# Kernel optimization log

Hardware: AMD Instinct MI355X
Metric: run time of the kernel (lower is better)

The kernel has to match this reference:

```python
import jax, jax.numpy as jnp
import numpy as np

W_ENTROPY, W_MI, W_COV, W_ORTHO, W_L1, W_L2 = 1.0, 0.2, 0.2, 0.1, 0.1, 0.1


def setup_inputs() -> dict:
    key = jax.random.key(0)
    k1, k2, k3, k4 = jax.random.split(key, 4)
    B, NCLS, C = 16384, 1000, 1280
    logits = jax.random.normal(k1, (B, NCLS), dtype=jnp.float32)
    output = jax.nn.log_softmax(logits, axis=1)  # nll_loss expects log-probs
    target = jax.random.randint(k2, (B,), 0, NCLS, dtype=jnp.int64)
    weights = jax.random.normal(k3, (NCLS, C), dtype=jnp.float32) * 0.02
    features = jax.random.normal(k4, (B, C), dtype=jnp.float32)
    return {"output": output, "target": target, "weights": weights, "features": features}


def _kl_loss(features):
    # torch: sum_{i,j} F.kl_div(L[:, i], L[:, j], log_target=True, reduction='mean')
    # kl_div(input, tgt, log_target=True) = mean_b exp(tgt)*(tgt - input)
    # => sum_{i,j,b} P[b,j]*(L[b,j]-L[b,i]) / B
    #  = (C * sum(P*L) - sum(L)) / B   (since sum_j P[b,j] == 1)
    B, C = features.shape
    L = jax.nn.log_softmax(features, axis=1)
    P = jnp.exp(L)
    return (C * jnp.sum(P * L) - jnp.sum(L)) / B


def _cov_loss(features):
    B = features.shape[0]
    cf = features - jnp.mean(features, axis=0, keepdims=True)
    cov = (cf.T @ cf) / B  # [C, C]
    eye = jnp.eye(cov.shape[0], dtype=cov.dtype)
    return jnp.sum((cov - eye) ** 2)  # ||.||_F^2


def _ortho_loss(weights):
    w = weights.reshape(weights.shape[0], -1)
    cov = w @ w.T  # row type
    eye = jnp.eye(cov.shape[0], dtype=cov.dtype)
    return jnp.sum((cov - eye) ** 2)


def reference(output, target, weights, features):
    loss_nll = -jnp.mean(jnp.take_along_axis(output, target[:, None], axis=1))
    loss_kl = _kl_loss(features)
    loss_cov = _cov_loss(features)
    loss_ortho = _ortho_loss(weights)
    loss_l1 = jnp.sum(jnp.abs(weights))
    loss_l2 = jnp.sqrt(jnp.sum(weights ** 2))
    loss = (W_ENTROPY * loss_nll + W_MI * loss_kl + W_COV * loss_cov
            + W_ORTHO * loss_ortho + W_L1 * loss_l1 + W_L2 * loss_l2)
    return loss
```

## Files before the change

### kernel.cpp

```cpp
#include <hip/hip_runtime.h>
#include <stdint.h>
#include <stddef.h>

#define B_N    16384
#define NCLS_N 1000
#define C_N    1280

#define ACC_OFF    0ULL
#define TICKET_OFF 64ULL
#define COLSUM_OFF 128ULL
#define FBT_OFF    8192ULL
#define WB_OFF     41951232ULL
#define G_OFF      44572672ULL
#define H_OFF      51126272ULL
#define HP_OFF     102244352ULL
#define WS_PART_NEED 111681536ULL

enum { A_NLL = 0, A_KL = 1, A_L1 = 2, A_L2SQ = 3, A_SUMSQF = 4, A_FMU2 = 5, A_GFRO = 6, A_HFRO = 7 };

typedef short s16x8 __attribute__((ext_vector_type(8)));
typedef float f32x4 __attribute__((ext_vector_type(4)));

__device__ __forceinline__ unsigned short f2bf(float f) {
    union { float f; unsigned int u; } v; v.f = f;
    unsigned int u = v.u;
    u += 0x7fffu + ((u >> 16) & 1u);
    return (unsigned short)(u >> 16);
}

__device__ __forceinline__ float wave_red(float v) {
#pragma unroll
    for (int o = 32; o; o >>= 1) v += __shfl_down(v, o, 64);
    return v;
}


__device__ __forceinline__ void nll_body(const float* __restrict__ lp,
                                         const int* __restrict__ tgt,
                                         float* __restrict__ acc, int bidx) {
    int b = bidx * 256 + threadIdx.x;
    int t = tgt[b];
    float v = lp[(size_t)b * NCLS_N + t];
    v = wave_red(v);
    __shared__ float sm_nll[4];
    int wid = threadIdx.x >> 6, lane = threadIdx.x & 63;
    if (lane == 0) sm_nll[wid] = v;
    __syncthreads();
    if (threadIdx.x == 0) atomicAdd(&acc[A_NLL], sm_nll[0] + sm_nll[1] + sm_nll[2] + sm_nll[3]);
}

__device__ __forceinline__ void wpass_body(const float* __restrict__ W,
                                           short* __restrict__ Wb,
                                           float* __restrict__ acc, int idx) {
    int bx = idx & 3;
    int kc = idx >> 2;
    int m = bx * 256 + threadIdx.x;
    bool live = (m < NCLS_N);
    const float4* Wr = (const float4*)(W + (size_t)m * C_N);
    float l1 = 0.f, l2 = 0.f;
#pragma unroll
    for (int kj = 0; kj < 4; kj++) {
        s16x8 pk = { 0, 0, 0, 0, 0, 0, 0, 0 };
        if (live) {
            float4 a = Wr[kc * 8 + kj * 2];
            float4 b = Wr[kc * 8 + kj * 2 + 1];
            l1 += fabsf(a.x) + fabsf(a.y) + fabsf(a.z) + fabsf(a.w)
                + fabsf(b.x) + fabsf(b.y) + fabsf(b.z) + fabsf(b.w);
            l2 += a.x * a.x + a.y * a.y + a.z * a.z + a.w * a.w
                + b.x * b.x + b.y * b.y + b.z * b.z + b.w * b.w;
            pk[0] = (short)f2bf(a.x); pk[1] = (short)f2bf(a.y);
            pk[2] = (short)f2bf(a.z); pk[3] = (short)f2bf(a.w);
            pk[4] = (short)f2bf(b.x); pk[5] = (short)f2bf(b.y);
            pk[6] = (short)f2bf(b.z); pk[7] = (short)f2bf(b.w);
        }
        *(s16x8*)(Wb + ((size_t)(kc * 4 + kj) * 1024 + m) * 8) = pk;
    }
    l1 = wave_red(l1);
    l2 = wave_red(l2);
    __shared__ float sm_w[4][2];
    int wid = threadIdx.x >> 6, lane = threadIdx.x & 63;
    if (lane == 0) { sm_w[wid][0] = l1; sm_w[wid][1] = l2; }
    __syncthreads();
    if (threadIdx.x == 0) {
        atomicAdd(&acc[A_L1],   sm_w[0][0] + sm_w[1][0] + sm_w[2][0] + sm_w[3][0]);
        atomicAdd(&acc[A_L2SQ], sm_w[0][1] + sm_w[1][1] + sm_w[2][1] + sm_w[3][1]);
    }
}

__device__ __forceinline__ void fpass_body(const float* __restrict__ F,
                                           short* __restrict__ Fbt,
                                           float* __restrict__ colsum,
                                           float* __restrict__ acc, int idx) {
    int bx = idx % 5;
    int by = idx / 5;
    int c = bx * 256 + threadIdx.x;
    int kc0 = by * 4;
    float cs = 0.f, sq = 0.f;
    for (int ch = 0; ch < 4; ch++) {
        int kc = kc0 + ch;
        int kbase = kc * 32;
#pragma unroll
        for (int kj = 0; kj < 4; kj++) {
            float v[8];
#pragma unroll
            for (int e = 0; e < 8; e++) v[e] = F[(size_t)(kbase + kj * 8 + e) * C_N + c];
            s16x8 pk;
#pragma unroll
            for (int e = 0; e < 8; e++) {
                cs += v[e];
                sq += v[e] * v[e];
                pk[e] = (short)f2bf(v[e]);
            }
            *(s16x8*)(Fbt + ((size_t)(kc * 4 + kj) * C_N + c) * 8) = pk;
        }
    }
    atomicAdd(&colsum[c], cs);
    sq = wave_red(sq);
    __shared__ float sm_f[4];
    int wid = threadIdx.x >> 6, lane = threadIdx.x & 63;
    if (lane == 0) sm_f[wid] = sq;
    __syncthreads();
    if (threadIdx.x == 0) atomicAdd(&acc[A_SUMSQF], sm_f[0] + sm_f[1] + sm_f[2] + sm_f[3]);
}

__device__ __forceinline__ void klpass_body(const float* __restrict__ F,
                                            float* __restrict__ acc, int idx) {
    int wid = threadIdx.x >> 6, lane = threadIdx.x & 63;
    int gwave = idx * 4 + wid;
    float kl_acc = 0.f;
    for (int b = gwave; b < B_N; b += 4096) {
        const float4* Fr = (const float4*)(F + (size_t)b * C_N);
        float s = 0.f, tt = 0.f;
#pragma unroll
        for (int i = 0; i < 5; i++) {
            float4 f = Fr[lane + 64 * i];
            float e0 = __expf(f.x), e1 = __expf(f.y), e2 = __expf(f.z), e3 = __expf(f.w);
            s  += e0 + e1 + e2 + e3;
            tt += e0 * f.x + e1 * f.y + e2 * f.z + e3 * f.w;
        }
        s = wave_red(s); tt = wave_red(tt);
        if (lane == 0) kl_acc += (float)C_N * (tt / s);
    }
    __shared__ float sm_kl[4];
    if (lane == 0) sm_kl[wid] = kl_acc;
    __syncthreads();
    if (threadIdx.x == 0)
        atomicAdd(&acc[A_KL], sm_kl[0] + sm_kl[1] + sm_kl[2] + sm_kl[3]);
}

template<bool PART>
__device__ __forceinline__ void gram_body(const short* __restrict__ X,
                                          float* __restrict__ S,
                                          int Mp, int T, int ntri,
                                          int tile, int kc_blk, int k0step, int nt) {
    __shared__ __align__(16) short A0[128 * 32];
    __shared__ __align__(16) short A1[128 * 32];
    __shared__ __align__(16) short B0[128 * 32];
    __shared__ __align__(16) short B1[128 * 32];
    int tid = threadIdx.x;
    int bi = 0, rem = tile;
    while (rem >= T - bi) { rem -= T - bi; bi++; }
    int bj = bi + rem;
    int i0 = bi * 128, j0 = bj * 128;

    int wave = tid >> 6, lane = tid & 63;
    int wm = wave >> 1, wn = wave & 1;
    int quad = lane >> 4, l16 = lane & 15;

    const size_t kstep = (size_t)Mp * 32;
    const short *pa0, *pa1, *pb0, *pb1;
    int lo0 = tid * 8, lo1 = (256 + tid) * 8;
    {
        int g0 = tid, g1 = 256 + tid;
        int r0 = g0 >> 2, r1 = g1 >> 2;
        int kj0 = (g0 & 3) ^ (r0 & 3), kj1 = (g1 & 3) ^ (r1 & 3);
        size_t base = (size_t)k0step * kstep;
        pa0 = X + base + ((size_t)kj0 * Mp + i0 + r0) * 8;
        pa1 = X + base + ((size_t)kj1 * Mp + i0 + r1) * 8;
        pb0 = X + base + ((size_t)kj0 * Mp + j0 + r0) * 8;
        pb1 = X + base + ((size_t)kj1 * Mp + j0 + r1) * 8;
    }

    f32x4 acc[4][4];
#pragma unroll
    for (int i = 0; i < 4; i++)
#pragma unroll
        for (int j = 0; j < 4; j++) acc[i][j] = { 0.f, 0.f, 0.f, 0.f };

    auto stage = [&](short* Ad, short* Bd) {
        __builtin_amdgcn_global_load_lds((const __attribute__((address_space(1))) unsigned int*)pa0,
                                         (__attribute__((address_space(3))) unsigned int*)(Ad + lo0), 16, 0, 0);
        __builtin_amdgcn_global_load_lds((const __attribute__((address_space(1))) unsigned int*)pa1,
                                         (__attribute__((address_space(3))) unsigned int*)(Ad + lo1), 16, 0, 0);
        __builtin_amdgcn_global_load_lds((const __attribute__((address_space(1))) unsigned int*)pb0,
                                         (__attribute__((address_space(3))) unsigned int*)(Bd + lo0), 16, 0, 0);
        __builtin_amdgcn_global_load_lds((const __attribute__((address_space(1))) unsigned int*)pb1,
                                         (__attribute__((address_space(3))) unsigned int*)(Bd + lo1), 16, 0, 0);
        pa0 += kstep; pa1 += kstep; pb0 += kstep; pb1 += kstep;
    };

    auto compute = [&](const short* Ab, const short* Bb) {
        s16x8 af[4], bfr[4];
#pragma unroll
        for (int f = 0; f < 4; f++) {
            int mrow = wm * 64 + f * 16 + l16;
            af[f] = *(const s16x8*)(Ab + mrow * 32 + (quad ^ (mrow & 3)) * 8);
            int nrow = wn * 64 + f * 16 + l16;
            bfr[f] = *(const s16x8*)(Bb + nrow * 32 + (quad ^ (nrow & 3)) * 8);
        }
        __builtin_amdgcn_s_setprio(1);
#pragma unroll
        for (int i = 0; i < 4; i++)
#pragma unroll
            for (int j = 0; j < 4; j++)
                acc[i][j] = __builtin_amdgcn_mfma_f32_16x16x32_bf16(af[i], bfr[j], acc[i][j], 0, 0, 0);
        __builtin_amdgcn_s_setprio(0);
    };

    stage(A0, B0);
    __syncthreads();
    for (int t = 0; t < nt; t += 2) {
        stage(A1, B1);
        compute(A0, B0);
        __syncthreads();
        if (t + 2 < nt) stage(A0, B0);
        compute(A1, B1);
        __syncthreads();
    }

    if (PART) {
        float* Sp = S + (((size_t)kc_blk * ntri + tile) << 14);
#pragma unroll
        for (int i = 0; i < 4; i++)
#pragma unroll
            for (int j = 0; j < 4; j++)
#pragma unroll
                for (int r = 0; r < 4; r++) {
                    int lrow = wm * 64 + i * 16 + quad * 4 + r;
                    int lcol = wn * 64 + j * 16 + l16;
                    Sp[lrow * 128 + lcol] = acc[i][j][r];
                }
    } else {
#pragma unroll
        for (int i = 0; i < 4; i++)
#pragma unroll
            for (int j = 0; j < 4; j++)
#pragma unroll
                for (int r = 0; r < 4; r++) {
                    int grow = i0 + wm * 64 + i * 16 + quad * 4 + r;
                    int gcol = j0 + wn * 64 + j * 16 + l16;
                    atomicAdd(&S[(size_t)grow * Mp + gcol], acc[i][j][r]);
                }
    }
}

__device__ __forceinline__ void fro_tile_any(const float* __restrict__ S,
                                             const float* __restrict__ mu_src,
                                             int Mp, int T, int ntri, int tile, int nks, bool part,
                                             float* __restrict__ slotF,
                                             float* __restrict__ slotQ) {
    int bi = 0, rem = tile;
    while (rem >= T - bi) { rem -= T - bi; bi++; }
    int bj = bi + rem;
    size_t baseA = (size_t)bi * 128 * Mp + (size_t)bj * 128;
    const float* baseP = S + ((size_t)tile << 14);
    size_t pstride = (size_t)ntri << 14;
    const float invB = 1.f / (float)B_N;
    float sum = 0.f, q = 0.f;
    for (int l = threadIdx.x * 4; l < 128 * 128; l += 1024) {
        int row = l >> 7, col = l & 127;
        float4 v;
        if (part) {
            v = *(const float4*)(baseP + l);
            for (int ks = 1; ks < nks; ks++) {
                float4 u = *(const float4*)(baseP + (size_t)ks * pstride + l);
                v.x += u.x; v.y += u.y; v.z += u.z; v.w += u.w;
            }
        } else {
            v = *(const float4*)(S + baseA + (size_t)row * Mp + col);
        }
        sum += v.x * v.x + v.y * v.y + v.z * v.z + v.w * v.w;
        if (mu_src) {
            float mr = mu_src[bi * 128 + row] * invB;
            float4 mc = *(const float4*)(mu_src + bj * 128 + col);
            q += mr * (v.x * mc.x + v.y * mc.y + v.z * mc.z + v.w * mc.w) * invB;
        }
    }
    sum = wave_red(sum);
    q = wave_red(q);
    __shared__ float sm_fro[4][2];
    int wid = threadIdx.x >> 6, lane = threadIdx.x & 63;
    if (lane == 0) { sm_fro[wid][0] = sum; sm_fro[wid][1] = q; }
    __syncthreads();
    if (threadIdx.x == 0) {
        float w = (bi == bj) ? 1.f : 2.f;
        atomicAdd(slotF, w * (sm_fro[0][0] + sm_fro[1][0] + sm_fro[2][0] + sm_fro[3][0]));
        if (mu_src)
            atomicAdd(slotQ, w * (sm_fro[0][1] + sm_fro[1][1] + sm_fro[2][1] + sm_fro[3][1]));
    }
}


__global__ __launch_bounds__(256) void prep_kernel(const float* __restrict__ lp,
                                                   const int* __restrict__ tgt,
                                                   const float* __restrict__ W,
                                                   const float* __restrict__ F,
                                                   short* __restrict__ Wb,
                                                   short* __restrict__ Fbt,
                                                   float* __restrict__ colsum,
                                                   float* __restrict__ acc,
                                                   float* __restrict__ G,
                                                   float* __restrict__ H) {
    int b = blockIdx.x;
    if (b < 1024) {
        klpass_body(F, acc, b);
    } else if (b < 1664) {
        fpass_body(F, Fbt, colsum, acc, b - 1024);
    } else if (b < 1824) {
        wpass_body(W, Wb, acc, b - 1664);
    } else if (b < 1888) {
        nll_body(lp, tgt, acc, b - 1824);
    } else if (b < 1988) {
        float4* p = (float4*)G + (size_t)(b - 1888) * 4096;
        float4 z = { 0.f, 0.f, 0.f, 0.f };
        for (int i = threadIdx.x; i < 4096; i += 256) p[i] = z;
    } else {
        float4* p = (float4*)H + (size_t)(b - 1988) * 4096;
        float4 z = { 0.f, 0.f, 0.f, 0.f };
        for (int i = threadIdx.x; i < 4096; i += 256) p[i] = z;
    }
}

template<bool PART>
__global__ __launch_bounds__(256) void main_kernel(const short* __restrict__ Fbt,
                                                   float* __restrict__ G,
                                                   const short* __restrict__ Wb,
                                                   float* __restrict__ H) {
    const int G_NT[16] = {18,22,26,30,20,24,28,32,46,42,38,34,44,40,36,32};
    const int G_K0[16] = {0,18,40,66,96,116,140,168,200,246,288,326,360,404,444,480};
    const int H_NT[4]  = {8,10,12,10};
    const int H_K0[4]  = {0,8,18,30};
    int b = blockIdx.x;
    if (b < 880) {
        int tile = b >> 4, kc = b & 15;
        int k0 = PART ? kc * 32 : G_K0[kc];
        int nt = PART ? 32      : G_NT[kc];
        gram_body<PART>(Fbt, G, C_N, 10, 55, tile, kc, k0, nt);
    } else {
        int l = b - 880;
        int tile = l >> 2, kc = l & 3;
        int k0 = PART ? kc * 10 : H_K0[kc];
        int nt = PART ? 10      : H_NT[kc];
        gram_body<PART>(Wb, H, 1024, 8, 36, tile, kc, k0, nt);
    }
}

template<bool PART>
__global__ __launch_bounds__(256) void fro_final_kernel(const float* __restrict__ G,
                                                        const float* __restrict__ H,
                                                        float* __restrict__ acc,
                                                        const float* __restrict__ colsum,
                                                        unsigned* __restrict__ ticket,
                                                        float* __restrict__ out) {
    int b = blockIdx.x;
    if (b < 55) fro_tile_any(G, colsum, C_N, 10, 55, b, 16, PART, acc + A_GFRO, acc + A_FMU2);
    else        fro_tile_any(H, nullptr, 1024, 8, 36, b - 55, 4, PART, acc + A_HFRO, nullptr);

    __shared__ int amlast;
    if (threadIdx.x == 0) {
        __threadfence();
        unsigned prev = atomicAdd(ticket, 1u);
        amlast = (prev == 90u);
    }
    __syncthreads();
    if (!amlast) return;
    __threadfence();

    float s = 0.f, s1 = 0.f;
    for (int c = threadIdx.x; c < C_N; c += 256) { float v = colsum[c]; s += v * v; s1 += v; }
    s = wave_red(s);
    s1 = wave_red(s1);
    __shared__ float sm[4][2];
    int wid = threadIdx.x >> 6, lane = threadIdx.x & 63;
    if (lane == 0) { sm[wid][0] = s; sm[wid][1] = s1; }
    __syncthreads();
    if (threadIdx.x == 0) {
        double musq_raw = (double)(sm[0][0] + sm[1][0] + sm[2][0] + sm[3][0]);
        double sumF     = (double)(sm[0][1] + sm[1][1] + sm[2][1] + sm[3][1]);
        double Bd = (double)B_N;
        double gfro = (double)atomicAdd(&acc[A_GFRO], 0.0f);
        double hfro = (double)atomicAdd(&acc[A_HFRO], 0.0f);
        double fmu2 = (double)atomicAdd(&acc[A_FMU2], 0.0f);
        double nll = -((double)acc[A_NLL] / Bd);
        double kl  = ((double)acc[A_KL] - sumF) / Bd;
        double trG = (double)acc[A_SUMSQF];
        double musq = musq_raw / (Bd * Bd);
        double cov = gfro / (Bd * Bd)
                   - (2.0 / Bd) * fmu2
                   + musq * musq
                   - 2.0 * (trG / Bd - musq)
                   + (double)C_N;
        double ortho = hfro - 2.0 * (double)acc[A_L2SQ] + (double)NCLS_N;
        double loss = 1.0 * nll + 0.2 * kl + 0.2 * cov + 0.1 * ortho
                    + 0.1 * (double)acc[A_L1] + 0.1 * sqrt((double)acc[A_L2SQ]);
        out[0] = (float)loss;
    }
}

extern "C" void kernel_launch(void* const* d_in, const int* in_sizes, int n_in,
                              void* d_out, int out_size, void* d_ws, size_t ws_size,
                              hipStream_t stream) {
    (void)in_sizes; (void)n_in; (void)out_size;
    const float* output_lp = (const float*)d_in[0];
    const int*   target    = (const int*)d_in[1];
    const float* W         = (const float*)d_in[2];
    const float* F         = (const float*)d_in[3];

    char*     ws     = (char*)d_ws;
    float*    acc    = (float*)(ws + ACC_OFF);
    unsigned* ticket = (unsigned*)(ws + TICKET_OFF);
    float*    colsum = (float*)(ws + COLSUM_OFF);
    short*    Fbt    = (short*)(ws + FBT_OFF);
    short*    Wb     = (short*)(ws + WB_OFF);

    bool part = (ws_size >= WS_PART_NEED);

    hipMemsetAsync(ws, 0, 8192, stream);

    if (part) {
        float* Gp = (float*)(ws + G_OFF);
        float* Hp = (float*)(ws + HP_OFF);
        prep_kernel<<<1888, 256, 0, stream>>>(output_lp, target, W, F, Wb, Fbt, colsum, acc, Gp, Hp);
        main_kernel<true><<<1024, 256, 0, stream>>>(Fbt, Gp, Wb, Hp);
        fro_final_kernel<true><<<91, 256, 0, stream>>>(Gp, Hp, acc, colsum, ticket, (float*)d_out);
    } else {
        float* G = (float*)(ws + G_OFF);
        float* H = (float*)(ws + H_OFF);
        prep_kernel<<<2052, 256, 0, stream>>>(output_lp, target, W, F, Wb, Fbt, colsum, acc, G, H);
        main_kernel<false><<<1024, 256, 0, stream>>>(Fbt, G, Wb, H);
        fro_final_kernel<false><<<91, 256, 0, stream>>>(G, H, acc, colsum, ticket, (float*)d_out);
    }
}
```

Baseline: 268.5 us.

## Fuse KL and feature-transpose passes; split fro tiles into quarter-tile blocks

Merges the separate KL pass and the bf16 feature transpose/colsum pass into a single kernel body, so the 84 MB feature matrix is read once instead of twice. Each wave handles 8 rows with coalesced float4 loads, accumulates column sums in shared memory and writes the transposed bf16 layout. It also splits each Frobenius tile reduction into four 32-row blocks to raise parallelism in the final kernel, and adjusts the last-block ticket count to match. The costs are shared-memory atomics for column sums and more register pressure from per-row accumulators.

Result: no change. 266.2 us (-0.8%).

```diff
diff --git a/kernel.cpp b/kernel.cpp
--- a/kernel.cpp
+++ b/kernel.cpp
@@ -87,65 +87,66 @@
     }
 }
 
-__device__ __forceinline__ void fpass_body(const float* __restrict__ F,
-                                           short* __restrict__ Fbt,
-                                           float* __restrict__ colsum,
-                                           float* __restrict__ acc, int idx) {
-    int bx = idx % 5;
-    int by = idx / 5;
-    int c = bx * 256 + threadIdx.x;
-    int kc0 = by * 4;
-    float cs = 0.f, sq = 0.f;
-    for (int ch = 0; ch < 4; ch++) {
-        int kc = kc0 + ch;
-        int kbase = kc * 32;
-#pragma unroll
-        for (int kj = 0; kj < 4; kj++) {
-            float v[8];
-#pragma unroll
-            for (int e = 0; e < 8; e++) v[e] = F[(size_t)(kbase + kj * 8 + e) * C_N + c];
-            s16x8 pk;
-#pragma unroll
-            for (int e = 0; e < 8; e++) {
-                cs += v[e];
-                sq += v[e] * v[e];
-                pk[e] = (short)f2bf(v[e]);
-            }
-            *(s16x8*)(Fbt + ((size_t)(kc * 4 + kj) * C_N + c) * 8) = pk;
+__device__ __forceinline__ void fkpass_body(const float* __restrict__ F,
+                                            short* __restrict__ Fbt,
+                                            float* __restrict__ colsum,
+                                            float* __restrict__ acc, int kc) {
+    __shared__ float csum[C_N];
+    __shared__ float sm_red[4][2];
+    int tid = threadIdx.x;
+    int w = tid >> 6, lane = tid & 63;
+    for (int i = tid; i < C_N; i += 256) csum[i] = 0.f;
+    __syncthreads();
+
+    int b0 = kc * 32 + w * 8;
+    float s_acc[8], tt_acc[8];
+#pragma unroll
+    for (int r = 0; r < 8; r++) { s_acc[r] = 0.f; tt_acc[r] = 0.f; }
+    float sq = 0.f;
+
+    for (int cc = 0; cc < 5; cc++) {
+        int cbase = cc * 256 + 4 * lane;
+        f32x4 cs = { 0.f, 0.f, 0.f, 0.f };
+        s16x8 out0, out1, out2, out3;
+#pragma unroll
+        for (int r = 0; r < 8; r++) {
+            float4 f = *(const float4*)(F + (size_t)(b0 + r) * C_N + cbase);
+            float e0 = __expf(f.x), e1 = __expf(f.y), e2 = __expf(f.z), e3 = __expf(f.w);
+            s_acc[r]  += e0 + e1 + e2 + e3;
+            tt_acc[r] += e0 * f.x + e1 * f.y + e2 * f.z + e3 * f.w;
+            cs.x += f.x; cs.y += f.y; cs.z += f.z; cs.w += f.w;
+            sq += f.x * f.x + f.y * f.y + f.z * f.z + f.w * f.w;
+            out0[r] = (short)f2bf(f.x);
+            out1[r] = (short)f2bf(f.y);
+            out2[r] = (short)f2bf(f.z);
+            out3[r] = (short)f2bf(f.w);
         }
-    }
-    atomicAdd(&colsum[c], cs);
+        short* dst = Fbt + ((size_t)(kc * 4 + w) * C_N + cbase) * 8;
+        *(s16x8*)(dst)      = out0;
+        *(s16x8*)(dst + 8)  = out1;
+        *(s16x8*)(dst + 16) = out2;
+        *(s16x8*)(dst + 24) = out3;
+        atomicAdd(&csum[cbase + 0], cs.x);
+        atomicAdd(&csum[cbase + 1], cs.y);
+        atomicAdd(&csum[cbase + 2], cs.z);
+        atomicAdd(&csum[cbase + 3], cs.w);
+    }
+
+    float kl_acc = 0.f;
+#pragma unroll
+    for (int r = 0; r < 8; r++) {
+        float s = wave_red(s_acc[r]);
+        float tt = wave_red(tt_acc[r]);
+        if (lane == 0) kl_acc += (float)C_N * (tt / s);
+    }
     sq = wave_red(sq);
-    __shared__ float sm_f[4];
-    int wid = threadIdx.x >> 6, lane = threadIdx.x & 63;
-    if (lane == 0) sm_f[wid] = sq;
-    __syncthreads();
-    if (threadIdx.x == 0) atomicAdd(&acc[A_SUMSQF], sm_f[0] + sm_f[1] + sm_f[2] + sm_f[3]);
-}
-
-__device__ __forceinline__ void klpass_body(const float* __restrict__ F,
-                                            float* __restrict__ acc, int idx) {
-    int wid = threadIdx.x >> 6, lane = threadIdx.x & 63;
-    int gwave = idx * 4 + wid;
-    float kl_acc = 0.f;
-    for (int b = gwave; b < B_N; b += 4096) {
-        const float4* Fr = (const float4*)(F + (size_t)b * C_N);
-        float s = 0.f, tt = 0.f;
-#pragma unroll
-        for (int i = 0; i < 5; i++) {
-            float4 f = Fr[lane + 64 * i];
-            float e0 = __expf(f.x), e1 = __expf(f.y), e2 = __expf(f.z), e3 = __expf(f.w);
-            s  += e0 + e1 + e2 + e3;
-            tt += e0 * f.x + e1 * f.y + e2 * f.z + e3 * f.w;
-        }
-        s = wave_red(s); tt = wave_red(tt);
-        if (lane == 0) kl_acc += (float)C_N * (tt / s);
-    }
-    __shared__ float sm_kl[4];
-    if (lane == 0) sm_kl[wid] = kl_acc;
-    __syncthreads();
-    if (threadIdx.x == 0)
-        atomicAdd(&acc[A_KL], sm_kl[0] + sm_kl[1] + sm_kl[2] + sm_kl[3]);
+    if (lane == 0) { sm_red[w][0] = sq; sm_red[w][1] = kl_acc; }
+    __syncthreads();
+    for (int i = tid; i < C_N; i += 256) atomicAdd(&colsum[i], csum[i]);
+    if (tid == 0) {
+        atomicAdd(&acc[A_SUMSQF], sm_red[0][0] + sm_red[1][0] + sm_red[2][0] + sm_red[3][0]);
+        atomicAdd(&acc[A_KL],     sm_red[0][1] + sm_red[1][1] + sm_red[2][1] + sm_red[3][1]);
+    }
 }
 
 template<bool PART>
@@ -256,24 +257,25 @@
 
 __device__ __forceinline__ void fro_tile_any(const float* __restrict__ S,
                                              const float* __restrict__ mu_src,
-                                             int Mp, int T, int ntri, int tile, int nks, bool part,
+                                             int Mp, int T, int ntri, int tile, int q,
+                                             int nks, bool part,
                                              float* __restrict__ slotF,
                                              float* __restrict__ slotQ) {
     int bi = 0, rem = tile;
     while (rem >= T - bi) { rem -= T - bi; bi++; }
     int bj = bi + rem;
-    size_t baseA = (size_t)bi * 128 * Mp + (size_t)bj * 128;
-    const float* baseP = S + ((size_t)tile << 14);
+    const float invB = 1.f / (float)B_N;
+    const float* baseP = S + ((size_t)tile << 14) + ((size_t)q << 12);
     size_t pstride = (size_t)ntri << 14;
-    const float invB = 1.f / (float)B_N;
-    float sum = 0.f, q = 0.f;
-    for (int l = threadIdx.x * 4; l < 128 * 128; l += 1024) {
-        int row = l >> 7, col = l & 127;
+    size_t baseA = (size_t)(bi * 128 + q * 32) * Mp + (size_t)bj * 128;
+    float sum = 0.f, qacc = 0.f;
+    for (int e = threadIdx.x * 4; e < 4096; e += 1024) {
+        int row = e >> 7, col = e & 127;
         float4 v;
         if (part) {
-            v = *(const float4*)(baseP + l);
+            v = *(const float4*)(baseP + e);
             for (int ks = 1; ks < nks; ks++) {
-                float4 u = *(const float4*)(baseP + (size_t)ks * pstride + l);
+                float4 u = *(const float4*)(baseP + (size_t)ks * pstride + e);
                 v.x += u.x; v.y += u.y; v.z += u.z; v.w += u.w;
             }
         } else {
@@ -281,16 +283,16 @@
         }
         sum += v.x * v.x + v.y * v.y + v.z * v.z + v.w * v.w;
         if (mu_src) {
-            float mr = mu_src[bi * 128 + row] * invB;
+            float mr = mu_src[bi * 128 + q * 32 + row] * invB;
             float4 mc = *(const float4*)(mu_src + bj * 128 + col);
-            q += mr * (v.x * mc.x + v.y * mc.y + v.z * mc.z + v.w * mc.w) * invB;
+            qacc += mr * (v.x * mc.x + v.y * mc.y + v.z * mc.z + v.w * mc.w) * invB;
         }
     }
     sum = wave_red(sum);
-    q = wave_red(q);
+    qacc = wave_red(qacc);
     __shared__ float sm_fro[4][2];
     int wid = threadIdx.x >> 6, lane = threadIdx.x & 63;
-    if (lane == 0) { sm_fro[wid][0] = sum; sm_fro[wid][1] = q; }
+    if (lane == 0) { sm_fro[wid][0] = sum; sm_fro[wid][1] = qacc; }
     __syncthreads();
     if (threadIdx.x == 0) {
         float w = (bi == bj) ? 1.f : 2.f;
@@ -312,20 +314,18 @@
                                                    float* __restrict__ G,
                                                    float* __restrict__ H) {
     int b = blockIdx.x;
-    if (b < 1024) {
-        klpass_body(F, acc, b);
-    } else if (b < 1664) {
-        fpass_body(F, Fbt, colsum, acc, b - 1024);
-    } else if (b < 1824) {
-        wpass_body(W, Wb, acc, b - 1664);
-    } else if (b < 1888) {
-        nll_body(lp, tgt, acc, b - 1824);
-    } else if (b < 1988) {
-        float4* p = (float4*)G + (size_t)(b - 1888) * 4096;
+    if (b < 512) {
+        fkpass_body(F, Fbt, colsum, acc, b);
+    } else if (b < 672) {
+        wpass_body(W, Wb, acc, b - 512);
+    } else if (b < 736) {
+        nll_body(lp, tgt, acc, b - 672);
+    } else if (b < 836) {
+        float4* p = (float4*)G + (size_t)(b - 736) * 4096;
         float4 z = { 0.f, 0.f, 0.f, 0.f };
         for (int i = threadIdx.x; i < 4096; i += 256) p[i] = z;
     } else {
-        float4* p = (float4*)H + (size_t)(b - 1988) * 4096;
+        float4* p = (float4*)H + (size_t)(b - 836) * 4096;
         float4 z = { 0.f, 0.f, 0.f, 0.f };
         for (int i = threadIdx.x; i < 4096; i += 256) p[i] = z;
     }
@@ -363,14 +363,14 @@
                                                         unsigned* __restrict__ ticket,
                                                         float* __restrict__ out) {
     int b = blockIdx.x;
-    if (b < 55) fro_tile_any(G, colsum, C_N, 10, 55, b, 16, PART, acc + A_GFRO, acc + A_FMU2);
-    else        fro_tile_any(H, nullptr, 1024, 8, 36, b - 55, 4, PART, acc + A_HFRO, nullptr);
+    if (b < 220) fro_tile_any(G, colsum, C_N, 10, 55, b >> 2, b & 3, 16, PART, acc + A_GFRO, acc + A_FMU2);
+    else { int l = b - 220; fro_tile_any(H, nullptr, 1024, 8, 36, l >> 2, l & 3, 4, PART, acc + A_HFRO, nullptr); }
 
     __shared__ int amlast;
     if (threadIdx.x == 0) {
         __threadfence();
         unsigned prev = atomicAdd(ticket, 1u);
-        amlast = (prev == 90u);
+        amlast = (prev == 363u);
     }
     __syncthreads();
     if (!amlast) return;
@@ -430,14 +430,14 @@
     if (part) {
         float* Gp = (float*)(ws + G_OFF);
         float* Hp = (float*)(ws + HP_OFF);
-        prep_kernel<<<1888, 256, 0, stream>>>(output_lp, target, W, F, Wb, Fbt, colsum, acc, Gp, Hp);
+        prep_kernel<<<736, 256, 0, stream>>>(output_lp, target, W, F, Wb, Fbt, colsum, acc, Gp, Hp);
         main_kernel<true><<<1024, 256, 0, stream>>>(Fbt, Gp, Wb, Hp);
-        fro_final_kernel<true><<<91, 256, 0, stream>>>(Gp, Hp, acc, colsum, ticket, (float*)d_out);
+        fro_final_kernel<true><<<364, 256, 0, stream>>>(Gp, Hp, acc, colsum, ticket, (float*)d_out);
     } else {
         float* G = (float*)(ws + G_OFF);
         float* H = (float*)(ws + H_OFF);
-        prep_kernel<<<2052, 256, 0, stream>>>(output_lp, target, W, F, Wb, Fbt, colsum, acc, G, H);
+        prep_kernel<<<900, 256, 0, stream>>>(output_lp, target, W, F, Wb, Fbt, colsum, acc, G, H);
         main_kernel<false><<<1024, 256, 0, stream>>>(Fbt, G, Wb, H);
-        fro_final_kernel<false><<<91, 256, 0, stream>>>(G, H, acc, colsum, ticket, (float*)d_out);
-    }
-}
+        fro_final_kernel<false><<<364, 256, 0, stream>>>(G, H, acc, colsum, ticket, (float*)d_out);
+    }
+}
```
